# Kernel optimization log

Hardware: AMD Instinct MI355X
Metric: run time of the kernel (lower is better)

Reference implementation:

```python
import jax, jax.numpy as jnp
import numpy as np

K_TOP = 2
N_HEADS = 4

def _ln(x, g, b, eps=1e-5):
    mu = x.mean(-1, keepdims=True)
    var = ((x - mu) ** 2).mean(-1, keepdims=True)
    return (x - mu) * jax.lax.rsqrt(var + eps) * g + b

def setup_inputs() -> dict:
    key = jax.random.key(0)
    ks = jax.random.split(key, 12)
    B, Na, dz, da = 1024, 32, 96, 32
    D = dz + da
    E, F, Hh, nr = 8, 1024, 512, 4
    s = 0.02
    rn = lambda k, sh: jax.random.normal(k, sh, jnp.float32) * s
    return dict(
        z=jax.random.normal(ks[0], (B, Na, dz), jnp.float32),
        a=jax.random.normal(ks[1], (B, Na, da), jnp.float32),
        w_gate=rn(ks[2], (Na * D, E)),
        w_in=rn(ks[3], (E, 3 * D, D)), b_in=jnp.zeros((E, 3 * D), jnp.float32),
        w_out=rn(ks[4], (E, D, D)), b_out=jnp.zeros((E, D), jnp.float32),
        ln1_g=jnp.ones((E, D), jnp.float32), ln1_b=jnp.zeros((E, D), jnp.float32),
        w1=rn(ks[5], (E, F, D)), b1=jnp.zeros((E, F), jnp.float32),
        w2=rn(ks[6], (E, D, F)), b2=jnp.zeros((E, D), jnp.float32),
        ln2_g=jnp.ones((E, D), jnp.float32), ln2_b=jnp.zeros((E, D), jnp.float32),
        head_w1=rn(ks[7], (Hh, Na * D)), head_b1=jnp.zeros((Hh,), jnp.float32),
        head_w2=rn(ks[8], (nr, Hh)), head_b2=jnp.zeros((nr,), jnp.float32),
    )

def reference(z, a, w_gate, w_in, b_in, w_out, b_out, ln1_g, ln1_b, w1, b1, w2, b2, ln2_g, ln2_b, head_w1, head_b1, head_w2, head_b2):
    B, Na, _ = z.shape
    x = jnp.concatenate([z, a], axis=-1)          # [B, Na, D]
    D = x.shape[-1]
    E = w_gate.shape[1]
    hd = D // N_HEADS
    x_flat = x.reshape(B, -1)                     # [B, Na*D]

    # --- NoisyTopKRouter (eval: clean logits only) ---
    logits = x_flat @ w_gate                      # [B, E]
    top_vals, top_idx = jax.lax.top_k(logits, min(K_TOP + 1, E))
    tk_gates = jax.nn.softmax(top_vals[:, :K_TOP], axis=1)
    gates = jnp.zeros_like(logits).at[jnp.arange(B)[:, None], top_idx[:, :K_TOP]].set(tk_gates)
    load = (gates > 0).sum(0).astype(jnp.float32)
    importance = gates.sum(0)
    cv2 = lambda v: jnp.var(v, ddof=1) / (jnp.mean(v) ** 2 + 1e-10)
    loss_bal = cv2(importance) + cv2(load) + jax.scipy.special.logsumexp(logits, axis=-1).mean()

    # --- expert (self-attn + FFN, pre/post-LN residual) ---
    def expert(p):
        wi, bi, wo, bo, g1, be1, W1, B1, W2, B2, g2, be2 = p
        qkv = x @ wi.T + bi                       # [B, Na, 3D]
        q, k_, v = jnp.split(qkv, 3, axis=-1)
        q = q.reshape(B, Na, N_HEADS, hd)
        k_ = k_.reshape(B, Na, N_HEADS, hd)
        v = v.reshape(B, Na, N_HEADS, hd)
        sc = jnp.einsum('bqhd,bkhd->bhqk', q, k_) / jnp.sqrt(jnp.float32(hd))
        att = jax.nn.softmax(sc, axis=-1)
        o = jnp.einsum('bhqk,bkhd->bqhd', att, v).reshape(B, Na, D)
        o = o @ wo.T + bo
        h = _ln(x + o, g1, be1)
        f = jax.nn.relu(h @ W1.T + B1) @ W2.T + B2
        return _ln(h + f, g2, be2)

    def body(y, p):
        *ep, gate_e = p                           # gate_e: [B]
        y = y + gate_e[:, None, None] * expert(tuple(ep))
        return y, None

    xs = (w_in, b_in, w_out, b_out, ln1_g, ln1_b, w1, b1, w2, b2, ln2_g, ln2_b, gates.T)
    y, _ = jax.lax.scan(body, jnp.zeros_like(x), xs)

    y_flat = y.reshape(B, -1)
    r = jax.nn.relu(y_flat @ head_w1.T + head_b1) @ head_w2.T + head_b2  # [B, n_r]
    return r, gates, loss_bal
```

## Files before the change

### kernel.cpp

```cpp
#include <hip/hip_runtime.h>
#include <math.h>


typedef short bf16x8 __attribute__((ext_vector_type(8)));
typedef float f32x4 __attribute__((ext_vector_type(4)));
typedef unsigned short u16;

#define MFMA(a, b, c) __builtin_amdgcn_mfma_f32_16x16x32_bf16((a), (b), (c), 0, 0, 0)

__device__ __forceinline__ u16 f2bf(float f) {
    unsigned int u = __float_as_uint(f);
    unsigned int r = u + 0x7FFFu + ((u >> 16) & 1u);
    return (u16)(r >> 16);
}
__device__ __forceinline__ float bf2f(u16 s) {
    return __uint_as_float(((unsigned int)s) << 16);
}

__global__ __launch_bounds__(256) void convert_kernel(
    const float* __restrict__ wi, const float* __restrict__ wo,
    const float* __restrict__ w1, const float* __restrict__ w2,
    const float* __restrict__ hw1,
    u16* __restrict__ wiB, u16* __restrict__ woB, u16* __restrict__ w1B,
    u16* __restrict__ w2B, u16* __restrict__ hw1B)
{
    int i4 = blockIdx.x * 256 + threadIdx.x;
    int e = i4 * 4;
    const float* s; u16* d; int off;
    if (e < 393216)       { s = wi;  d = wiB;  off = e; }
    else if (e < 524288)  { s = wo;  d = woB;  off = e - 393216; }
    else if (e < 1572864) { s = w1;  d = w1B;  off = e - 524288; }
    else if (e < 2621440) { s = w2;  d = w2B;  off = e - 1572864; }
    else                  { s = hw1; d = hw1B; off = e - 2621440; }
    float4 v = *(const float4*)(s + off);
    ushort4 o;
    o.x = f2bf(v.x); o.y = f2bf(v.y); o.z = f2bf(v.z); o.w = f2bf(v.w);
    *(ushort4*)(d + off) = o;
}

__global__ __launch_bounds__(256) void router_kernel(
    const float* __restrict__ z, const float* __restrict__ a,
    const float* __restrict__ wg,
    float* __restrict__ gates_out, float* __restrict__ lse_ws,
    int* __restrict__ topi, float* __restrict__ topg)
{
    __shared__ float red[256][9];
    const int b = blockIdx.x, t = threadIdx.x;
    float acc[8];
#pragma unroll
    for (int e = 0; e < 8; ++e) acc[e] = 0.f;
#pragma unroll
    for (int i = 0; i < 16; ++i) {
        int f = i * 256 + t;
        int n = f >> 7, d = f & 127;
        float xv = (d < 96) ? z[(b * 32 + n) * 96 + d]
                            : a[(b * 32 + n) * 32 + d - 96];
        const float* wr = wg + f * 8;
#pragma unroll
        for (int e = 0; e < 8; ++e) acc[e] += xv * wr[e];
    }
#pragma unroll
    for (int e = 0; e < 8; ++e) red[t][e] = acc[e];
    __syncthreads();
    for (int s = 128; s; s >>= 1) {
        if (t < s) {
#pragma unroll
            for (int e = 0; e < 8; ++e) red[t][e] += red[t + s][e];
        }
        __syncthreads();
    }
    if (t == 0) {
        float L[8];
#pragma unroll
        for (int e = 0; e < 8; ++e) L[e] = red[0][e];
        int i0 = 0;
#pragma unroll
        for (int e = 1; e < 8; ++e) if (L[e] > L[i0]) i0 = e;
        int i1 = -1; float v1 = -3.0e38f;
#pragma unroll
        for (int e = 0; e < 8; ++e) if (e != i0 && L[e] > v1) { v1 = L[e]; i1 = e; }
        float e1 = expf(v1 - L[i0]);
        float inv = 1.f / (1.f + e1);
        float g0 = inv, g1 = e1 * inv;
#pragma unroll
        for (int e = 0; e < 8; ++e)
            gates_out[b * 8 + e] = (e == i0) ? g0 : ((e == i1) ? g1 : 0.f);
        float m = L[i0];
        float se = 0.f;
#pragma unroll
        for (int e = 0; e < 8; ++e) se += expf(L[e] - m);
        lse_ws[b] = m + logf(se);
        topi[b * 2 + 0] = i0; topi[b * 2 + 1] = i1;
        topg[b * 2 + 0] = g0; topg[b * 2 + 1] = g1;
    }
}

__global__ __launch_bounds__(1024) void build_loss_kernel(
    const int* __restrict__ topi, const float* __restrict__ topg,
    const float* __restrict__ lse,
    int* __restrict__ cnts, int* __restrict__ ent, int* __restrict__ meta,
    int* __restrict__ metaF, float* __restrict__ out_loss)
{
    __shared__ int sc_[8];
    __shared__ int toff[8];
    __shared__ int toffF[8];
    __shared__ float red[9][1024];
    const int t = threadIdx.x;
    if (t < 8) sc_[t] = 0;
    __syncthreads();
    int e0 = topi[t * 2], e1 = topi[t * 2 + 1];
    float g0 = topg[t * 2], g1 = topg[t * 2 + 1];
    int p0 = atomicAdd(&sc_[e0], 1);
    ent[e0 * 2048 + p0] = t * 2;
    int p1 = atomicAdd(&sc_[e1], 1);
    ent[e1 * 2048 + p1] = t * 2 + 1;
#pragma unroll
    for (int e = 0; e < 8; ++e)
        red[e][t] = ((e == e0) ? g0 : 0.f) + ((e == e1) ? g1 : 0.f);
    red[8][t] = lse[t];
    __syncthreads();
    for (int s = 512; s; s >>= 1) {
        if (t < s) {
#pragma unroll
            for (int q = 0; q < 9; ++q) red[q][t] += red[q][t + s];
        }
        __syncthreads();
    }
    if (t == 0) {
        int off = 0, offF = 0;
        for (int e = 0; e < 8; ++e) {
            toff[e] = off;   off  += (sc_[e] + 1) >> 1;
            toffF[e] = offF; offF += (sc_[e] + 3) >> 2;
        }
        meta[0] = off;
        metaF[0] = offF;
        float cvv[2];
        for (int p = 0; p < 2; ++p) {
            float v[8], sum = 0.f;
            for (int e = 0; e < 8; ++e) {
                v[e] = p ? (float)sc_[e] : red[e][0];
                sum += v[e];
            }
            float mean = sum * (1.f / 8.f);
            float var = 0.f;
            for (int e = 0; e < 8; ++e) { float d = v[e] - mean; var += d * d; }
            var *= (1.f / 7.f);
            cvv[p] = var / (mean * mean + 1e-10f);
        }
        out_loss[0] = cvv[0] + cvv[1] + red[8][0] * (1.f / 1024.f);
    }
    __syncthreads();
    if (t < 8) {
        cnts[t] = sc_[t];
        int ntl = (sc_[t] + 1) >> 1, o = toff[t];
        for (int j = 0; j < ntl; ++j) {
            meta[1 + 2 * (o + j)] = t;
            meta[2 + 2 * (o + j)] = j * 2;
        }
        int ntlF = (sc_[t] + 3) >> 2, oF = toffF[t];
        for (int j = 0; j < ntlF; ++j) {
            metaF[1 + 2 * (oF + j)] = t;
            metaF[2 + 2 * (oF + j)] = j * 4;
        }
    }
}

#define SM_X 0
#define SM_Q 16384
#define SM_K 32768
#define SM_V 49152
#define SM_TOT 65536
#define PS_OFF 0
#define PQ_OFF 1024
#define MU_OFF 2048
#define RS_OFF 2304
#define NTILES 1028

__device__ __forceinline__ int tsw(int row, int col) {
    return row * 256 + ((col * 2) ^ ((row & 7) << 4));
}
__device__ __forceinline__ int vsw(int row, int col) {
    return row * 128 + ((col * 2) ^ ((row & 7) << 4));
}

__global__ __launch_bounds__(512, 2) void attn_kernel(
    const float* __restrict__ z, const float* __restrict__ a,
    const u16* __restrict__ wiBF, const float* __restrict__ b_in,
    const u16* __restrict__ woBF, const float* __restrict__ b_out,
    const float* __restrict__ ln1g, const float* __restrict__ ln1b,
    const int* __restrict__ cnts, const int* __restrict__ meta,
    const int* __restrict__ ent,
    u16* __restrict__ h1g)
{
    __shared__ __align__(16) char sm[SM_TOT];
    const int n_tiles = meta[0];
    const int bid = blockIdx.x;
    if (bid >= n_tiles) return;
    const int e = meta[1 + 2 * bid], base = meta[2 + 2 * bid];
    const int cnt = cnts[e];

    const int t = threadIdx.x;
    const int w = t >> 6, l = t & 63, l16 = l & 15, lk = l >> 4;
    const int ke = lk * 8;
    const int wr = w >> 2, wc = w & 3;
    const f32x4 zv = {0.f, 0.f, 0.f, 0.f};

    int bs[2];
#pragma unroll
    for (int i = 0; i < 2; ++i) {
        int gi = base + i;
        int idx = (gi < cnt) ? gi : (cnt - 1);
        bs[i] = ent[e * 2048 + idx];
    }

#pragma unroll
    for (int i = 0; i < 2; ++i) {
        int cid = i * 512 + t;
        int row = cid >> 4;
        int cb = (cid & 15) * 8;
        int b_ = bs[row >> 5] >> 1;
        int n = row & 31;
        float4 p0, p1;
        if (cb < 96) {
            const float* zp = z + ((size_t)b_ * 32 + n) * 96 + cb;
            p0 = *(const float4*)zp; p1 = *(const float4*)(zp + 4);
        } else {
            const float* ap = a + ((size_t)b_ * 32 + n) * 32 + (cb - 96);
            p0 = *(const float4*)ap; p1 = *(const float4*)(ap + 4);
        }
        bf16x8 pk;
        pk[0] = (short)f2bf(p0.x); pk[1] = (short)f2bf(p0.y);
        pk[2] = (short)f2bf(p0.z); pk[3] = (short)f2bf(p0.w);
        pk[4] = (short)f2bf(p1.x); pk[5] = (short)f2bf(p1.y);
        pk[6] = (short)f2bf(p1.z); pk[7] = (short)f2bf(p1.w);
        *(bf16x8*)(sm + SM_X + tsw(row, cb)) = pk;
    }
    __syncthreads();

    {
        f32x4 acc[2][6];
#pragma unroll
        for (int mt = 0; mt < 2; ++mt)
#pragma unroll
            for (int q = 0; q < 6; ++q) acc[mt][q] = zv;
#pragma unroll
        for (int ks = 0; ks < 4; ++ks) {
            bf16x8 af[2];
#pragma unroll
            for (int mt = 0; mt < 2; ++mt) {
                int R = wr * 32 + mt * 16 + l16;
                af[mt] = *(const bf16x8*)(sm + SM_X + tsw(R, ks * 32 + ke));
            }
#pragma unroll
            for (int q = 0; q < 6; ++q) {
                int j = wc * 96 + q * 16 + l16;
                bf16x8 bb = *(const bf16x8*)(wiBF + e * 49152 + j * 128 + ks * 32 + ke);
#pragma unroll
                for (int mt = 0; mt < 2; ++mt) acc[mt][q] = MFMA(af[mt], bb, acc[mt][q]);
            }
        }
#pragma unroll
        for (int q = 0; q < 6; ++q) {
            int C = wc * 96 + q * 16 + l16;
            float bj = b_in[e * 384 + C];
#pragma unroll
            for (int mt = 0; mt < 2; ++mt)
#pragma unroll
                for (int i = 0; i < 4; ++i) {
                    int R = wr * 32 + mt * 16 + lk * 4 + i;
                    u16 val = f2bf(acc[mt][q][i] + bj);
                    if (C < 128) {
                        *(u16*)(sm + SM_Q + tsw(R, C)) = val;
                    } else if (C < 256) {
                        *(u16*)(sm + SM_K + tsw(R, C - 128)) = val;
                    } else {
                        *(u16*)(sm + SM_V + vsw(C - 256, R)) = val;
                    }
                }
        }
    }
    __syncthreads();

    {
        const int tok = w >> 2, hb = (w & 3) * 32;
        const float scale = 0.17677669529663687f;
        bf16x8 qa[2], kf[2];
#pragma unroll
        for (int mt = 0; mt < 2; ++mt) {
            int R = tok * 32 + mt * 16 + l16;
            qa[mt] = *(const bf16x8*)(sm + SM_Q + tsw(R, hb + ke));
            kf[mt] = *(const bf16x8*)(sm + SM_K + tsw(R, hb + ke));
        }
        f32x4 sc[2][2];
        sc[0][0] = MFMA(qa[0], kf[0], zv); sc[0][1] = MFMA(qa[0], kf[1], zv);
        sc[1][0] = MFMA(qa[1], kf[0], zv); sc[1][1] = MFMA(qa[1], kf[1], zv);
#pragma unroll
        for (int mt = 0; mt < 2; ++mt)
#pragma unroll
            for (int i = 0; i < 4; ++i) {
                float v0 = sc[mt][0][i] * scale, v1 = sc[mt][1][i] * scale;
                float m = fmaxf(v0, v1);
                m = fmaxf(m, __shfl_xor(m, 1)); m = fmaxf(m, __shfl_xor(m, 2));
                m = fmaxf(m, __shfl_xor(m, 4)); m = fmaxf(m, __shfl_xor(m, 8));
                float e0 = __expf(v0 - m), e1 = __expf(v1 - m);
                float ssum = e0 + e1;
                ssum += __shfl_xor(ssum, 1); ssum += __shfl_xor(ssum, 2);
                ssum += __shfl_xor(ssum, 4); ssum += __shfl_xor(ssum, 8);
                float inv = 1.f / ssum;
                int row = mt * 16 + lk * 4 + i;
                char* pb = sm + SM_X + w * 2048 + row * 64;
                int sw = (row & 3) << 4;
                *(u16*)(pb + ((l16 * 2) ^ sw)) = f2bf(e0 * inv);
                *(u16*)(pb + (((16 + l16) * 2) ^ sw)) = f2bf(e1 * inv);
            }
        bf16x8 pa[2];
#pragma unroll
        for (int mt = 0; mt < 2; ++mt) {
            int row = mt * 16 + l16;
            pa[mt] = *(const bf16x8*)(sm + SM_X + w * 2048 + row * 64 +
                                      ((ke * 2) ^ ((row & 3) << 4)));
        }
        f32x4 o[2][2];
#pragma unroll
        for (int nt = 0; nt < 2; ++nt) {
            int rv = hb + nt * 16 + l16;
            bf16x8 vb = *(const bf16x8*)(sm + SM_V + vsw(rv, tok * 32 + ke));
            o[0][nt] = MFMA(pa[0], vb, zv);
            o[1][nt] = MFMA(pa[1], vb, zv);
        }
#pragma unroll
        for (int mt = 0; mt < 2; ++mt)
#pragma unroll
            for (int nt = 0; nt < 2; ++nt)
#pragma unroll
                for (int i = 0; i < 4; ++i) {
                    int R = tok * 32 + mt * 16 + lk * 4 + i;
                    int C = hb + nt * 16 + l16;
                    *(u16*)(sm + SM_Q + tsw(R, C)) = f2bf(o[mt][nt][i]);
                }
    }
    __syncthreads();

    {
        f32x4 pr[2][2];
        pr[0][0] = zv; pr[0][1] = zv; pr[1][0] = zv; pr[1][1] = zv;
#pragma unroll
        for (int ks = 0; ks < 4; ++ks) {
            bf16x8 af[2];
#pragma unroll
            for (int mt = 0; mt < 2; ++mt) {
                int R = wr * 32 + mt * 16 + l16;
                af[mt] = *(const bf16x8*)(sm + SM_Q + tsw(R, ks * 32 + ke));
            }
#pragma unroll
            for (int nt = 0; nt < 2; ++nt) {
                int j = wc * 32 + nt * 16 + l16;
                bf16x8 bb = *(const bf16x8*)(woBF + e * 16384 + j * 128 + ks * 32 + ke);
                pr[0][nt] = MFMA(af[0], bb, pr[0][nt]);
                pr[1][nt] = MFMA(af[1], bb, pr[1][nt]);
            }
        }
        int C0 = wc * 32 + l16, C1 = C0 + 16;
        float bo0 = b_out[e * 128 + C0];
        float bo1 = b_out[e * 128 + C1];
        int b_ = bs[wr] >> 1;
#pragma unroll
        for (int mt = 0; mt < 2; ++mt)
#pragma unroll
            for (int i = 0; i < 4; ++i) {
                int R = wr * 32 + mt * 16 + lk * 4 + i;
                int n = R & 31;
                float x0 = (C0 < 96) ? z[((size_t)b_ * 32 + n) * 96 + C0]
                                     : a[((size_t)b_ * 32 + n) * 32 + C0 - 96];
                float x1 = (C1 < 96) ? z[((size_t)b_ * 32 + n) * 96 + C1]
                                     : a[((size_t)b_ * 32 + n) * 32 + C1 - 96];
                float u0 = pr[mt][0][i] + bo0 + x0;
                float u1v = pr[mt][1][i] + bo1 + x1;
                *(u16*)(sm + SM_K + tsw(R, C0)) = f2bf(u0);
                *(u16*)(sm + SM_K + tsw(R, C1)) = f2bf(u1v);
                float s = u0 + u1v;
                float q = u0 * u0 + u1v * u1v;
                s += __shfl_xor(s, 1); q += __shfl_xor(q, 1);
                s += __shfl_xor(s, 2); q += __shfl_xor(q, 2);
                s += __shfl_xor(s, 4); q += __shfl_xor(q, 4);
                s += __shfl_xor(s, 8); q += __shfl_xor(q, 8);
                if (l16 == 0) {
                    *(float*)(sm + SM_X + PS_OFF + (R * 4 + wc) * 4) = s;
                    *(float*)(sm + SM_X + PQ_OFF + (R * 4 + wc) * 4) = q;
                }
            }
    }
    __syncthreads();
    if (t < 64) {
        float s = 0.f, q = 0.f;
#pragma unroll
        for (int c = 0; c < 4; ++c) {
            s += *(const float*)(sm + SM_X + PS_OFF + (t * 4 + c) * 4);
            q += *(const float*)(sm + SM_X + PQ_OFF + (t * 4 + c) * 4);
        }
        float mu = s * (1.f / 128.f);
        float var = q * (1.f / 128.f) - mu * mu;
        *(float*)(sm + SM_X + MU_OFF + t * 4) = mu;
        *(float*)(sm + SM_X + RS_OFF + t * 4) = rsqrtf(var + 1e-5f);
    }
    __syncthreads();
    {
        int r_ = t >> 3, c0 = (t & 7) * 16;
        float mu_ = *(const float*)(sm + SM_X + MU_OFF + r_ * 4);
        float rs_ = *(const float*)(sm + SM_X + RS_OFF + r_ * 4);
#pragma unroll
        for (int j4 = 0; j4 < 2; ++j4) {
            int cb = c0 + j4 * 8;
            bf16x8* p = (bf16x8*)(sm + SM_K + tsw(r_, cb));
            bf16x8 vch = *p;
#pragma unroll
            for (int jj = 0; jj < 8; ++jj) {
                int c = cb + jj;
                float f = (bf2f((u16)vch[jj]) - mu_) * rs_ * ln1g[e * 128 + c] + ln1b[e * 128 + c];
                vch[jj] = (short)f2bf(f);
            }
            *p = vch;
        }
    }
    __syncthreads();
#pragma unroll
    for (int i = 0; i < 2; ++i) {
        int cid = i * 512 + t;
        int r_ = cid >> 4, cb = (cid & 15) * 8;
        int code = bs[r_ >> 5];
        u16* dst = h1g + (size_t)code * 4096 + (r_ & 31) * 128 + cb;
        *(bf16x8*)dst = *(const bf16x8*)(sm + SM_K + tsw(r_, cb));
    }
}

#define FH 0
#define FF 32768
#define FPS 65536
#define FPQ 67584
#define FMU 69632
#define FRS 70144
#define F_TOT 70656
#define NF_TILES 520

__global__ __launch_bounds__(512, 2) void ffn_kernel(
    const u16* __restrict__ h1g,
    const u16* __restrict__ w1BF, const float* __restrict__ b1,
    const u16* __restrict__ w2BF, const float* __restrict__ b2,
    const float* __restrict__ ln2g, const float* __restrict__ ln2b,
    const float* __restrict__ topg, const int* __restrict__ cnts,
    const int* __restrict__ metaF, const int* __restrict__ ent,
    u16* __restrict__ ybf)
{
    __shared__ __align__(16) char sm[F_TOT];
    const int nf = metaF[0];
    const int bid = blockIdx.x;
    if (bid >= nf) return;
    const int e = metaF[1 + 2 * bid], base = metaF[2 + 2 * bid];
    const int cnt = cnts[e];

    const int t = threadIdx.x;
    const int w = t >> 6, l = t & 63, l16 = l & 15, lk = l >> 4;
    const int ke = lk * 8;
    const int wr = w >> 2, wc = w & 3;
    const f32x4 zv = {0.f, 0.f, 0.f, 0.f};

    int code4[4]; float gg4[4];
#pragma unroll
    for (int i = 0; i < 4; ++i) {
        int gi = base + i;
        int idx = (gi < cnt) ? gi : (cnt - 1);
        code4[i] = ent[e * 2048 + idx];
        gg4[i] = topg[code4[i]];
    }

#pragma unroll
    for (int it = 0; it < 4; ++it) {
        int cid = it * 512 + t;
        int row = cid >> 4, cb = (cid & 15) * 8;
        int code = code4[row >> 5];
        *(bf16x8*)(sm + FH + tsw(row, cb)) =
            *(const bf16x8*)(h1g + (size_t)code * 4096 + (row & 31) * 128 + cb);
    }
    __syncthreads();

    f32x4 facc[4][2];
#pragma unroll
    for (int mt = 0; mt < 4; ++mt) { facc[mt][0] = zv; facc[mt][1] = zv; }

    for (int c = 0; c < 8; ++c) {
        f32x4 a1[4][2];
#pragma unroll
        for (int mt = 0; mt < 4; ++mt) { a1[mt][0] = zv; a1[mt][1] = zv; }
#pragma unroll
        for (int ks = 0; ks < 4; ++ks) {
            bf16x8 af[4];
#pragma unroll
            for (int mt = 0; mt < 4; ++mt) {
                int R = wr * 64 + mt * 16 + l16;
                af[mt] = *(const bf16x8*)(sm + FH + tsw(R, ks * 32 + ke));
            }
#pragma unroll
            for (int nt = 0; nt < 2; ++nt) {
                int j = c * 128 + wc * 32 + nt * 16 + l16;
                bf16x8 bb = *(const bf16x8*)(w1BF + e * 131072 + j * 128 + ks * 32 + ke);
#pragma unroll
                for (int mt = 0; mt < 4; ++mt) a1[mt][nt] = MFMA(af[mt], bb, a1[mt][nt]);
            }
        }
        __syncthreads();
#pragma unroll
        for (int nt = 0; nt < 2; ++nt) {
            int C = wc * 32 + nt * 16 + l16;
            float bv = b1[e * 1024 + c * 128 + C];
#pragma unroll
            for (int mt = 0; mt < 4; ++mt)
#pragma unroll
                for (int i = 0; i < 4; ++i) {
                    int R = wr * 64 + mt * 16 + lk * 4 + i;
                    *(u16*)(sm + FF + tsw(R, C)) = f2bf(fmaxf(a1[mt][nt][i] + bv, 0.f));
                }
        }
        __syncthreads();
#pragma unroll
        for (int ks = 0; ks < 4; ++ks) {
            bf16x8 af[4];
#pragma unroll
            for (int mt = 0; mt < 4; ++mt) {
                int R = wr * 64 + mt * 16 + l16;
                af[mt] = *(const bf16x8*)(sm + FF + tsw(R, ks * 32 + ke));
            }
#pragma unroll
            for (int nt = 0; nt < 2; ++nt) {
                int j = wc * 32 + nt * 16 + l16;
                bf16x8 bb = *(const bf16x8*)(w2BF + e * 131072 + j * 1024 +
                                             c * 128 + ks * 32 + ke);
#pragma unroll
                for (int mt = 0; mt < 4; ++mt) facc[mt][nt] = MFMA(af[mt], bb, facc[mt][nt]);
            }
        }
    }
    __syncthreads();

    {
        int C0 = wc * 32 + l16, C1 = C0 + 16;
        float b20 = b2[e * 128 + C0];
        float b21 = b2[e * 128 + C1];
#pragma unroll
        for (int mt = 0; mt < 4; ++mt)
#pragma unroll
            for (int i = 0; i < 4; ++i) {
                int R = wr * 64 + mt * 16 + lk * 4 + i;
                float h0 = bf2f(*(const u16*)(sm + FH + tsw(R, C0)));
                float h1v = bf2f(*(const u16*)(sm + FH + tsw(R, C1)));
                float u0 = facc[mt][0][i] + b20 + h0;
                float u1v = facc[mt][1][i] + b21 + h1v;
                *(u16*)(sm + FF + tsw(R, C0)) = f2bf(u0);
                *(u16*)(sm + FF + tsw(R, C1)) = f2bf(u1v);
                float s = u0 + u1v;
                float q = u0 * u0 + u1v * u1v;
                s += __shfl_xor(s, 1); q += __shfl_xor(q, 1);
                s += __shfl_xor(s, 2); q += __shfl_xor(q, 2);
                s += __shfl_xor(s, 4); q += __shfl_xor(q, 4);
                s += __shfl_xor(s, 8); q += __shfl_xor(q, 8);
                if (l16 == 0) {
                    *(float*)(sm + FPS + (R * 4 + wc) * 4) = s;
                    *(float*)(sm + FPQ + (R * 4 + wc) * 4) = q;
                }
            }
    }
    __syncthreads();
    if (t < 128) {
        float s = 0.f, q = 0.f;
#pragma unroll
        for (int c = 0; c < 4; ++c) {
            s += *(const float*)(sm + FPS + (t * 4 + c) * 4);
            q += *(const float*)(sm + FPQ + (t * 4 + c) * 4);
        }
        float mu = s * (1.f / 128.f);
        float var = q * (1.f / 128.f) - mu * mu;
        *(float*)(sm + FMU + t * 4) = mu;
        *(float*)(sm + FRS + t * 4) = rsqrtf(var + 1e-5f);
    }
    __syncthreads();
#pragma unroll
    for (int it = 0; it < 4; ++it) {
        int cid = it * 512 + t;
        int row = cid >> 4, cb = (cid & 15) * 8;
        float mu = *(const float*)(sm + FMU + row * 4);
        float rs = *(const float*)(sm + FRS + row * 4);
        int ei = row >> 5;
        float gm = gg4[ei];
        int code = code4[ei];
        int tok = code >> 1, slot = code & 1;
        bf16x8 v = *(const bf16x8*)(sm + FF + tsw(row, cb));
        bf16x8 o;
#pragma unroll
        for (int jj = 0; jj < 8; ++jj) {
            int cc = cb + jj;
            float f = (bf2f((u16)v[jj]) - mu) * rs * ln2g[e * 128 + cc] + ln2b[e * 128 + cc];
            o[jj] = (short)f2bf(gm * f);
        }
        *(bf16x8*)(ybf + (size_t)(slot * 1024 + tok) * 4096 + (row & 31) * 128 + cb) = o;
    }
}

__global__ __launch_bounds__(256) void combine_kernel(
    u16* __restrict__ y0, const u16* __restrict__ y1)
{
    int i = (blockIdx.x * 256 + threadIdx.x) * 8;
    bf16x8 a = *(const bf16x8*)(y0 + i);
    bf16x8 b = *(const bf16x8*)(y1 + i);
    bf16x8 o;
#pragma unroll
    for (int j = 0; j < 8; ++j)
        o[j] = (short)f2bf(bf2f((u16)a[j]) + bf2f((u16)b[j]));
    *(bf16x8*)(y0 + i) = o;
}

__global__ __launch_bounds__(256) void head1_mfma(
    const u16* __restrict__ y_bf, const u16* __restrict__ hw1BF,
    const float* __restrict__ hb1, float* __restrict__ h_act)
{
    const int t = threadIdx.x, w = t >> 6, l = t & 63, l16 = l & 15, lk = l >> 4;
    const int ke = lk * 8;
    const int mb = blockIdx.x * 32, cb = blockIdx.y * 64 + w * 16;
    const f32x4 zv = {0.f, 0.f, 0.f, 0.f};
    f32x4 acc[2]; acc[0] = zv; acc[1] = zv;
    const u16* arow0 = y_bf + (size_t)(mb + l16) * 4096;
    const u16* arow1 = y_bf + (size_t)(mb + 16 + l16) * 4096;
    const u16* brow  = hw1BF + (size_t)(cb + l16) * 4096;
    for (int k0 = 0; k0 < 4096; k0 += 32) {
        bf16x8 a0 = *(const bf16x8*)(arow0 + k0 + ke);
        bf16x8 a1 = *(const bf16x8*)(arow1 + k0 + ke);
        bf16x8 bb = *(const bf16x8*)(brow + k0 + ke);
        acc[0] = MFMA(a0, bb, acc[0]);
        acc[1] = MFMA(a1, bb, acc[1]);
    }
    int col = cb + l16;
    float bv = hb1[col];
#pragma unroll
    for (int mt = 0; mt < 2; ++mt)
#pragma unroll
        for (int i = 0; i < 4; ++i) {
            int row = mb + mt * 16 + lk * 4 + i;
            h_act[(size_t)row * 512 + col] = fmaxf(acc[mt][i] + bv, 0.f);
        }
}

__global__ __launch_bounds__(64) void head2_kernel(
    const float* __restrict__ h_act, const float* __restrict__ w2,
    const float* __restrict__ b2, float* __restrict__ r)
{
    const int b = blockIdx.x, t = threadIdx.x;
    float a0 = 0.f, a1 = 0.f, a2 = 0.f, a3 = 0.f;
    for (int h = t; h < 512; h += 64) {
        float hv = h_act[b * 512 + h];
        a0 += hv * w2[h];
        a1 += hv * w2[512 + h];
        a2 += hv * w2[1024 + h];
        a3 += hv * w2[1536 + h];
    }
#pragma unroll
    for (int off = 32; off; off >>= 1) {
        a0 += __shfl_down(a0, off);
        a1 += __shfl_down(a1, off);
        a2 += __shfl_down(a2, off);
        a3 += __shfl_down(a3, off);
    }
    if (t == 0) {
        r[b * 4 + 0] = a0 + b2[0];
        r[b * 4 + 1] = a1 + b2[1];
        r[b * 4 + 2] = a2 + b2[2];
        r[b * 4 + 3] = a3 + b2[3];
    }
}

extern "C" void kernel_launch(void* const* d_in, const int* in_sizes, int n_in,
                              void* d_out, int out_size, void* d_ws, size_t ws_size,
                              hipStream_t stream) {
    const float* z    = (const float*)d_in[0];
    const float* a    = (const float*)d_in[1];
    const float* wg   = (const float*)d_in[2];
    const float* w_in = (const float*)d_in[3];
    const float* b_in = (const float*)d_in[4];
    const float* w_o  = (const float*)d_in[5];
    const float* b_o  = (const float*)d_in[6];
    const float* l1g  = (const float*)d_in[7];
    const float* l1b  = (const float*)d_in[8];
    const float* w1   = (const float*)d_in[9];
    const float* b1   = (const float*)d_in[10];
    const float* w2   = (const float*)d_in[11];
    const float* b2   = (const float*)d_in[12];
    const float* l2g  = (const float*)d_in[13];
    const float* l2b  = (const float*)d_in[14];
    const float* hw1  = (const float*)d_in[15];
    const float* hb1  = (const float*)d_in[16];
    const float* hw2  = (const float*)d_in[17];
    const float* hb2  = (const float*)d_in[18];

    float* out = (float*)d_out;
    float* r_out     = out;
    float* gates_out = out + 4096;
    float* loss_out  = out + 12288;

    char* W = (char*)d_ws;
    u16*   wiBF  = (u16*)(W + 0);
    u16*   woBF  = (u16*)(W + 786432);
    u16*   w1BF  = (u16*)(W + 1048576);
    u16*   w2BF  = (u16*)(W + 3145728);
    u16*   hw1BF = (u16*)(W + 5242880);
    u16*   ybf   = (u16*)(W + 9437184);
    u16*   h1g   = (u16*)(W + 26214400);
    float* h_act = (float*)(W + 42991616);
    float* lse   = (float*)(W + 45088768);
    float* topg  = (float*)(W + 45092864);
    int*   topi  = (int*)  (W + 45101056);
    int*   cnts  = (int*)  (W + 45109248);
    int*   meta  = (int*)  (W + 45109376);
    int*   metaF = (int*)  (W + 45117696);
    int*   ent   = (int*)  (W + 45126016);

    convert_kernel<<<4608, 256, 0, stream>>>(w_in, w_o, w1, w2, hw1,
                                             wiBF, woBF, w1BF, w2BF, hw1BF);
    router_kernel<<<1024, 256, 0, stream>>>(z, a, wg, gates_out, lse, topi, topg);
    build_loss_kernel<<<1, 1024, 0, stream>>>(topi, topg, lse, cnts, ent, meta,
                                              metaF, loss_out);
    attn_kernel<<<NTILES, 512, 0, stream>>>(z, a, wiBF, b_in, woBF, b_o,
        l1g, l1b, cnts, meta, ent, h1g);
    ffn_kernel<<<NF_TILES, 512, 0, stream>>>(h1g, w1BF, b1, w2BF, b2,
        l2g, l2b, topg, cnts, metaF, ent, ybf);
    combine_kernel<<<2048, 256, 0, stream>>>(ybf, ybf + 4194304);
    head1_mfma<<<dim3(32, 8), 256, 0, stream>>>(ybf, hw1BF, hb1, h_act);
    head2_kernel<<<1024, 64, 0, stream>>>(h_act, hw2, hb2, r_out);
}
```

Measured before the change: 329.5 us.

## Prefetch FFN weight fragments into registers across barriers in expert FFN loop

```diff
diff --git a/kernel.cpp b/kernel.cpp
--- a/kernel.cpp
+++ b/kernel.cpp
@@ -7,6 +7,14 @@
 typedef unsigned short u16;
 
 #define MFMA(a, b, c) __builtin_amdgcn_mfma_f32_16x16x32_bf16((a), (b), (c), 0, 0, 0)
+
+#define BARX() do { \
+    asm volatile("s_waitcnt lgkmcnt(0)" ::: "memory"); \
+    __builtin_amdgcn_s_barrier(); \
+    __builtin_amdgcn_sched_barrier(0); \
+} while (0)
+
+#define PIN(x) asm volatile("" :: "v"(x))
 
 __device__ __forceinline__ u16 f2bf(float f) {
     unsigned int u = __float_as_uint(f);
@@ -481,11 +489,20 @@
         *(bf16x8*)(sm + FH + tsw(row, cb)) =
             *(const bf16x8*)(h1g + (size_t)code * 4096 + (row & 31) * 128 + cb);
     }
-    __syncthreads();
+    BARX();
 
     f32x4 facc[4][2];
 #pragma unroll
     for (int mt = 0; mt < 4; ++mt) { facc[mt][0] = zv; facc[mt][1] = zv; }
+
+    bf16x8 w1f[2][4];
+#pragma unroll
+    for (int nt = 0; nt < 2; ++nt)
+#pragma unroll
+        for (int ks = 0; ks < 4; ++ks) {
+            int j = wc * 32 + nt * 16 + l16;
+            w1f[nt][ks] = *(const bf16x8*)(w1BF + e * 131072 + j * 128 + ks * 32 + ke);
+        }
 
     for (int c = 0; c < 8; ++c) {
         f32x4 a1[4][2];
@@ -500,14 +517,26 @@
                 af[mt] = *(const bf16x8*)(sm + FH + tsw(R, ks * 32 + ke));
             }
 #pragma unroll
-            for (int nt = 0; nt < 2; ++nt) {
-                int j = c * 128 + wc * 32 + nt * 16 + l16;
-                bf16x8 bb = *(const bf16x8*)(w1BF + e * 131072 + j * 128 + ks * 32 + ke);
-#pragma unroll
-                for (int mt = 0; mt < 4; ++mt) a1[mt][nt] = MFMA(af[mt], bb, a1[mt][nt]);
-            }
-        }
-        __syncthreads();
+            for (int nt = 0; nt < 2; ++nt)
+#pragma unroll
+                for (int mt = 0; mt < 4; ++mt)
+                    a1[mt][nt] = MFMA(af[mt], w1f[nt][ks], a1[mt][nt]);
+        }
+        bf16x8 w2f[2][4];
+#pragma unroll
+        for (int nt = 0; nt < 2; ++nt)
+#pragma unroll
+            for (int ks = 0; ks < 4; ++ks) {
+                int j = wc * 32 + nt * 16 + l16;
+                w2f[nt][ks] = *(const bf16x8*)(w2BF + e * 131072 + j * 1024 +
+                                               c * 128 + ks * 32 + ke);
+            }
+#pragma unroll
+        for (int nt = 0; nt < 2; ++nt)
+#pragma unroll
+            for (int ks = 0; ks < 4; ++ks) PIN(w2f[nt][ks]);
+
+        BARX();
 #pragma unroll
         for (int nt = 0; nt < 2; ++nt) {
             int C = wc * 32 + nt * 16 + l16;
@@ -520,7 +549,20 @@
                     *(u16*)(sm + FF + tsw(R, C)) = f2bf(fmaxf(a1[mt][nt][i] + bv, 0.f));
                 }
         }
-        __syncthreads();
+        if (c < 7) {
+#pragma unroll
+            for (int nt = 0; nt < 2; ++nt)
+#pragma unroll
+                for (int ks = 0; ks < 4; ++ks) {
+                    int j = (c + 1) * 128 + wc * 32 + nt * 16 + l16;
+                    w1f[nt][ks] = *(const bf16x8*)(w1BF + e * 131072 + j * 128 + ks * 32 + ke);
+                }
+#pragma unroll
+            for (int nt = 0; nt < 2; ++nt)
+#pragma unroll
+                for (int ks = 0; ks < 4; ++ks) PIN(w1f[nt][ks]);
+        }
+        BARX();
 #pragma unroll
         for (int ks = 0; ks < 4; ++ks) {
             bf16x8 af[4];
@@ -530,16 +572,13 @@
                 af[mt] = *(const bf16x8*)(sm + FF + tsw(R, ks * 32 + ke));
             }
 #pragma unroll
-            for (int nt = 0; nt < 2; ++nt) {
-                int j = wc * 32 + nt * 16 + l16;
-                bf16x8 bb = *(const bf16x8*)(w2BF + e * 131072 + j * 1024 +
-                                             c * 128 + ks * 32 + ke);
-#pragma unroll
-                for (int mt = 0; mt < 4; ++mt) facc[mt][nt] = MFMA(af[mt], bb, facc[mt][nt]);
-            }
-        }
-    }
-    __syncthreads();
+            for (int nt = 0; nt < 2; ++nt)
+#pragma unroll
+                for (int mt = 0; mt < 4; ++mt)
+                    facc[mt][nt] = MFMA(af[mt], w2f[nt][ks], facc[mt][nt]);
+        }
+    }
+    BARX();
 
     {
         int C0 = wc * 32 + l16, C1 = C0 + 16;
```

After: 350.3 us. 1.06x slower.
